# Kernel tuning notes

Hardware: AMD Instinct MI355X
Metric: run time of the kernel (lower is better)

Reference implementation:

```python
import jax, jax.numpy as jnp
import numpy as np

N_ATOMS = 512
N_SAMPLES = 2 ** 15  # 32768
N_ITER = 64


def time_domain_to_real(x):
    # rfft then concat(real, imag) along last dim -> length 2*(N//2+1)
    s = jnp.fft.rfft(x, axis=-1)
    return jnp.concatenate([s.real, s.imag], axis=-1)


def real_to_time_domain(x):
    half = x.shape[-1] // 2
    c = x[..., :half] + 1j * x[..., half:]
    return jnp.fft.irfft(c, axis=-1)  # n = 2*(half-1) = N_SAMPLES


def setup_inputs() -> dict:
    key = jax.random.key(0)
    k1, k2 = jax.random.split(key)
    x = jax.random.normal(k1, (64, 1, N_SAMPLES), dtype=jnp.float32)
    # learned atoms, initialized exactly as in Model.__init__
    env = jnp.linspace(1.0, 0.0, N_SAMPLES, dtype=jnp.float32) ** 12
    atoms_td = jax.random.uniform(k2, (1, N_ATOMS, N_SAMPLES), dtype=jnp.float32,
                                  minval=-0.01, maxval=0.01) * env[None, None, :]
    atoms = time_domain_to_real(atoms_td)  # (1, N_ATOMS, 32770)
    return {"x": x, "atoms": atoms}


def reference(x, atoms):
    xr = time_domain_to_real(x)            # (B, 1, L), L = 32770
    an = atoms / jnp.linalg.norm(atoms, axis=-1, keepdims=True)  # unit_norm over last axis
    an = an[0]                             # (A, L)
    res0 = xr[:, 0, :]                     # (B, L)
    rec0 = jnp.zeros_like(res0)

    def step(carry, _):
        res, rec = carry
        # sum(atoms * residual, -1) == dot products -> avoid (B,A,L) intermediate
        dots = jnp.einsum('bl,al->ba', res, an)      # (B, A)
        idx = jnp.argmax(dots, axis=1)               # (B,)
        best = an[idx] * res                         # take_along_dim(corr) == atoms[idx]*res
        return (res - best, rec + best), None

    (res, rec), _ = jax.lax.scan(step, (res0, rec0), None, length=N_ITER)
    reconstruction = real_to_time_domain(rec[:, None, :])  # (B, 1, N_SAMPLES)
    return reconstruction, res[:, None, :]
```

## Files before the change

kernel.cpp:

```cpp
#include <hip/hip_runtime.h>
#include <math.h>

#define NSAMP 32768
#define MH    16384
#define LFREQ 32770
#define NRE   16385
#define NB    64
#define NA    512
#define NITER 64
#define RSTR  32772

#define KPS    33280
#define NSL    64
#define BN2    128
#define USLICE 8
#define NCH    4097

typedef __attribute__((ext_vector_type(8))) short bf16x8;
typedef __attribute__((ext_vector_type(8))) unsigned short u16x8;
typedef __attribute__((ext_vector_type(4))) float f32x4;

__device__ __forceinline__ int rev4_14(int v) {
  unsigned r = __brev((unsigned)v) >> 18;
  r = ((r & 0x1555u) << 1) | ((r >> 1) & 0x1555u);
  return (int)r;
}

__device__ __forceinline__ unsigned short f2bf(float f) {
  unsigned u = __float_as_uint(f);
  u = (u + 0x7fffu + ((u >> 16) & 1u)) >> 16;
  return (unsigned short)u;
}
__device__ __forceinline__ float bf2f(unsigned short h) {
  return __uint_as_float(((unsigned)h) << 16);
}

__device__ __forceinline__ float2 cmul(float2 a, float2 b) {
  return make_float2(a.x * b.x - a.y * b.y, a.x * b.y + a.y * b.x);
}

__global__ __launch_bounds__(1024) void fft_fwd_kernel(const float* __restrict__ x,
                                                       float* __restrict__ res0,
                                                       unsigned short* __restrict__ resH,
                                                       unsigned short* __restrict__ resL) {
  extern __shared__ float2 s[];
  const int b = blockIdx.x, t = threadIdx.x;
  const float2* xrow = (const float2*)(x + (size_t)b * NSAMP);
  for (int m = t; m < MH; m += 1024) s[m] = xrow[rev4_14(m)];
  __syncthreads();
  for (int st = 0; st < 7; ++st) {
    const int q = 1 << (2 * st);
    const float fac = 6.283185307179586f / (float)(4 * q);
    for (int j = t; j < MH / 4; j += 1024) {
      const int blk = j >> (2 * st), pos = j & (q - 1);
      const int i0 = (blk << (2 * st + 2)) + pos;
      float sn, cs; __sincosf(fac * (float)pos, &sn, &cs);
      const float2 w1 = make_float2(cs, -sn);
      const float2 w2 = cmul(w1, w1);
      const float2 w3 = cmul(w2, w1);
      const float2 a0 = s[i0], a1 = s[i0 + q], a2 = s[i0 + 2 * q], a3 = s[i0 + 3 * q];
      const float2 x1 = cmul(w1, a1), x2 = cmul(w2, a2), x3 = cmul(w3, a3);
      const float2 s0 = make_float2(a0.x + x2.x, a0.y + x2.y);
      const float2 s1 = make_float2(a0.x - x2.x, a0.y - x2.y);
      const float2 t0 = make_float2(x1.x + x3.x, x1.y + x3.y);
      const float2 t1 = make_float2(x1.x - x3.x, x1.y - x3.y);
      s[i0]         = make_float2(s0.x + t0.x, s0.y + t0.y);
      s[i0 + q]     = make_float2(s1.x + t1.y, s1.y - t1.x);
      s[i0 + 2 * q] = make_float2(s0.x - t0.x, s0.y - t0.y);
      s[i0 + 3 * q] = make_float2(s1.x - t1.y, s1.y + t1.x);
    }
    __syncthreads();
  }
  float* rr = res0 + (size_t)b * RSTR;
  unsigned short* hrow = resH + (size_t)b * KPS;
  unsigned short* lrow = resL + (size_t)b * KPS;
  const float fac2 = 6.283185307179586f / (float)NSAMP;
  for (int k = t; k < MH; k += 1024) {
    if (k == 0) {
      const float2 z0 = s[0];
      const float dc = z0.x + z0.y, ny = z0.x - z0.y;
      rr[0] = dc;   rr[NRE] = 0.f;
      rr[MH] = ny;  rr[NRE + MH] = 0.f;
      unsigned short h;
      h = f2bf(dc); hrow[0] = h;  lrow[0] = f2bf(dc - bf2f(h));
      h = f2bf(ny); hrow[MH] = h; lrow[MH] = f2bf(ny - bf2f(h));
      hrow[NRE] = 0; lrow[NRE] = 0;
      hrow[NRE + MH] = 0; lrow[NRE + MH] = 0;
    } else {
      const float2 zk = s[k], zm = s[MH - k];
      const float xer = 0.5f * (zk.x + zm.x), xei = 0.5f * (zk.y - zm.y);
      const float p = 0.5f * (zk.y + zm.y);
      const float q = -0.5f * (zk.x - zm.x);
      float sn, cs; __sincosf(fac2 * (float)k, &sn, &cs);
      const float vr = xer + cs * p + sn * q;
      const float vi = xei + cs * q - sn * p;
      rr[k]       = vr;
      rr[NRE + k] = vi;
      unsigned short h;
      h = f2bf(vr); hrow[k] = h;       lrow[k] = f2bf(vr - bf2f(h));
      h = f2bf(vi); hrow[NRE + k] = h; lrow[NRE + k] = f2bf(vi - bf2f(h));
    }
  }
}

__global__ __launch_bounds__(1024) void fft_inv_kernel(const float* __restrict__ rec,
                                                       float* __restrict__ out) {
  extern __shared__ float2 s[];
  const int b = blockIdx.x, t = threadIdx.x;
  const float* rr = rec + (size_t)b * RSTR;
  const float fac2 = 6.283185307179586f / (float)NSAMP;
  for (int m = t; m < MH; m += 1024) {
    const int k = rev4_14(m);
    float2 z;
    if (k == 0) {
      const float a0 = rr[0], aM = rr[MH];
      z = make_float2(0.5f * (a0 + aM), 0.5f * (a0 - aM));
    } else {
      const float xr_ = rr[k],       xi_ = rr[NRE + k];
      const float mr  = rr[MH - k],  mi  = rr[NRE + MH - k];
      const float xer = 0.5f * (xr_ + mr), xei = 0.5f * (xi_ - mi);
      const float er  = 0.5f * (xr_ - mr), ei  = 0.5f * (xi_ + mi);
      float sn, cs; __sincosf(fac2 * (float)k, &sn, &cs);
      const float xor_ = cs * er - sn * ei;
      const float xoi  = cs * ei + sn * er;
      z = make_float2(xer - xoi, xei + xor_);
    }
    s[m] = z;
  }
  __syncthreads();
  for (int st = 0; st < 7; ++st) {
    const int q = 1 << (2 * st);
    const float fac = 6.283185307179586f / (float)(4 * q);
    for (int j = t; j < MH / 4; j += 1024) {
      const int blk = j >> (2 * st), pos = j & (q - 1);
      const int i0 = (blk << (2 * st + 2)) + pos;
      float sn, cs; __sincosf(fac * (float)pos, &sn, &cs);
      const float2 w1 = make_float2(cs, sn);
      const float2 w2 = cmul(w1, w1);
      const float2 w3 = cmul(w2, w1);
      const float2 a0 = s[i0], a1 = s[i0 + q], a2 = s[i0 + 2 * q], a3 = s[i0 + 3 * q];
      const float2 x1 = cmul(w1, a1), x2 = cmul(w2, a2), x3 = cmul(w3, a3);
      const float2 s0 = make_float2(a0.x + x2.x, a0.y + x2.y);
      const float2 s1 = make_float2(a0.x - x2.x, a0.y - x2.y);
      const float2 t0 = make_float2(x1.x + x3.x, x1.y + x3.y);
      const float2 t1 = make_float2(x1.x - x3.x, x1.y - x3.y);
      s[i0]         = make_float2(s0.x + t0.x, s0.y + t0.y);
      s[i0 + q]     = make_float2(s1.x - t1.y, s1.y + t1.x);
      s[i0 + 2 * q] = make_float2(s0.x - t0.x, s0.y - t0.y);
      s[i0 + 3 * q] = make_float2(s1.x + t1.y, s1.y - t1.x);
    }
    __syncthreads();
  }
  const float inv = 1.0f / (float)MH;
  float2* orow = (float2*)(out + (size_t)b * NSAMP);
  for (int m = t; m < MH; m += 1024) {
    const float2 z = s[m];
    orow[m] = make_float2(z.x * inv, z.y * inv);
  }
}

__global__ __launch_bounds__(256) void atom_norm_kernel(const float* __restrict__ atoms,
                                                        float* __restrict__ rnorm,
                                                        float* __restrict__ anv) {
  const int a = blockIdx.x, t = threadIdx.x;
  const float2* row2 = (const float2*)(atoms + (size_t)a * LFREQ);
  float ss = 0.f;
  for (int i = t; i < LFREQ / 2; i += 256) {
    const float2 v = row2[i];
    ss += v.x * v.x + v.y * v.y;
  }
  __shared__ float red[256];
  red[t] = ss; __syncthreads();
  for (int st = 128; st > 0; st >>= 1) {
    if (t < st) red[t] += red[t + st];
    __syncthreads();
  }
  if (t == 0) {
    const float rn = 1.0f / sqrtf(red[0]);
    rnorm[a] = rn;
    anv[a] = atoms[(size_t)a * LFREQ + 32768] * rn;
  }
}

__global__ __launch_bounds__(256) void an_bf16_kernel(const float* __restrict__ atoms,
                                                      const float* __restrict__ rnorm,
                                                      unsigned short* __restrict__ anH,
                                                      unsigned short* __restrict__ anL) {
  const int quarter = blockIdx.x;
  const int a = blockIdx.y;
  const int t = threadIdx.x;
  const float rn = rnorm[a];
  const float* row = atoms + (size_t)a * LFREQ;
  unsigned short* hrow = anH + (size_t)a * KPS;
  unsigned short* lrow = anL + (size_t)a * KPS;
  const int c0 = quarter * 1040;
  const int c1 = min(c0 + 1040, KPS / 8);
  for (int c = c0 + t; c < c1; c += 256) {
    const int k0 = c * 8;
    float v[8];
    if (k0 + 8 <= LFREQ) {
      #pragma unroll
      for (int e = 0; e < 4; ++e) {
        const float2 p = *(const float2*)(row + k0 + 2 * e);
        v[2 * e] = p.x; v[2 * e + 1] = p.y;
      }
    } else {
      #pragma unroll
      for (int e = 0; e < 8; ++e) v[e] = (k0 + e < LFREQ) ? row[k0 + e] : 0.f;
    }
    u16x8 hv, lv;
    #pragma unroll
    for (int e = 0; e < 8; ++e) {
      const float sv = v[e] * rn;
      const unsigned short h = f2bf(sv);
      hv[e] = h;
      lv[e] = f2bf(sv - bf2f(h));
    }
    *(u16x8*)(hrow + k0) = hv;
    *(u16x8*)(lrow + k0) = lv;
  }
}

__global__ __launch_bounds__(512) void dots_mfma_kernel(const unsigned short* __restrict__ resH,
                                                        const unsigned short* __restrict__ resL,
                                                        const unsigned short* __restrict__ anH,
                                                        const unsigned short* __restrict__ anL,
                                                        float* __restrict__ partials) {
  __shared__ char smem[98304];
  const int slice = blockIdx.x;
  const int atile = blockIdx.y;
  const int t = threadIdx.x;
  const int w = t >> 6, l = t & 63;
  const int bh = w >> 2, aq = w & 3;
  const int kc0 = slice * 512;

  f32x4 acc00 = {0.f,0.f,0.f,0.f}, acc01 = acc00, acc10 = acc00, acc11 = acc00;

#define STAGE(cc, bb)                                                                     \
  {                                                                                       \
    const int kc = kc0 + (cc) * 64;                                                       \
    _Pragma("unroll")                                                                     \
    for (int j = 0; j < 6; ++j) {                                                         \
      const int u = w * 6 + j;                                                            \
      const unsigned short* gt = (u < 8) ? resH : (u < 16) ? resL : (u < 32) ? anH : anL; \
      const int base = (u < 8) ? 0 : (u < 16) ? 8192 : (u < 32) ? 16384 : 32768;          \
      const int usec = u - ((u < 8) ? 0 : (u < 16) ? 8 : (u < 32) ? 16 : 32);             \
      const int row0 = (u < 16) ? 0 : atile * BN2;                                        \
      const int rt = usec >> 1, kk = usec & 1;                                            \
      const unsigned short* g = gt + (size_t)(row0 + rt * 16 + (l & 15)) * KPS            \
                                + kc + kk * 32 + (l >> 4) * 8;                            \
      char* d = smem + (bb) * 49152 + base + usec * 1024 + l * 16;                        \
      __builtin_amdgcn_global_load_lds((const __attribute__((address_space(1))) void*)g,  \
                                       (__attribute__((address_space(3))) void*)d,        \
                                       16, 0, 0);                                        \
    }                                                                                     \
  }

#define COMPUTE(bb)                                                                      \
  {                                                                                       \
    const char* base = smem + (bb) * 49152;                                               \
    _Pragma("unroll")                                                                     \
    for (int kk = 0; kk < 2; ++kk) {                                                      \
      const bf16x8 aH0 = *(const bf16x8*)(base + ((bh * 2 + 0) * 2 + kk) * 1024 + l * 16);\
      const bf16x8 aH1 = *(const bf16x8*)(base + ((bh * 2 + 1) * 2 + kk) * 1024 + l * 16);\
      const bf16x8 aL0 = *(const bf16x8*)(base + 8192 + ((bh * 2 + 0) * 2 + kk) * 1024 + l * 16);\
      const bf16x8 aL1 = *(const bf16x8*)(base + 8192 + ((bh * 2 + 1) * 2 + kk) * 1024 + l * 16);\
      const bf16x8 bH0 = *(const bf16x8*)(base + 16384 + ((aq * 2 + 0) * 2 + kk) * 1024 + l * 16);\
      const bf16x8 bH1 = *(const bf16x8*)(base + 16384 + ((aq * 2 + 1) * 2 + kk) * 1024 + l * 16);\
      const bf16x8 bL0 = *(const bf16x8*)(base + 32768 + ((aq * 2 + 0) * 2 + kk) * 1024 + l * 16);\
      const bf16x8 bL1 = *(const bf16x8*)(base + 32768 + ((aq * 2 + 1) * 2 + kk) * 1024 + l * 16);\
      acc00 = __builtin_amdgcn_mfma_f32_16x16x32_bf16(aH0, bH0, acc00, 0, 0, 0);          \
      acc01 = __builtin_amdgcn_mfma_f32_16x16x32_bf16(aH0, bH1, acc01, 0, 0, 0);          \
      acc10 = __builtin_amdgcn_mfma_f32_16x16x32_bf16(aH1, bH0, acc10, 0, 0, 0);          \
      acc11 = __builtin_amdgcn_mfma_f32_16x16x32_bf16(aH1, bH1, acc11, 0, 0, 0);          \
      acc00 = __builtin_amdgcn_mfma_f32_16x16x32_bf16(aH0, bL0, acc00, 0, 0, 0);          \
      acc01 = __builtin_amdgcn_mfma_f32_16x16x32_bf16(aH0, bL1, acc01, 0, 0, 0);          \
      acc10 = __builtin_amdgcn_mfma_f32_16x16x32_bf16(aH1, bL0, acc10, 0, 0, 0);          \
      acc11 = __builtin_amdgcn_mfma_f32_16x16x32_bf16(aH1, bL1, acc11, 0, 0, 0);          \
      acc00 = __builtin_amdgcn_mfma_f32_16x16x32_bf16(aL0, bH0, acc00, 0, 0, 0);          \
      acc01 = __builtin_amdgcn_mfma_f32_16x16x32_bf16(aL0, bH1, acc01, 0, 0, 0);          \
      acc10 = __builtin_amdgcn_mfma_f32_16x16x32_bf16(aL1, bH0, acc10, 0, 0, 0);          \
      acc11 = __builtin_amdgcn_mfma_f32_16x16x32_bf16(aL1, bH1, acc11, 0, 0, 0);          \
    }                                                                                     \
  }

  STAGE(0, 0);
  #pragma unroll
  for (int c = 0; c < 8; ++c) {
    const int buf = c & 1;
    if (c < 7) {
      STAGE(c + 1, buf ^ 1);
      asm volatile("s_waitcnt vmcnt(6)" ::: "memory");
    } else {
      asm volatile("s_waitcnt vmcnt(0)" ::: "memory");
    }
    __builtin_amdgcn_s_barrier();
    __builtin_amdgcn_sched_barrier(0);
    COMPUTE(buf);
    __builtin_amdgcn_sched_barrier(0);
    __builtin_amdgcn_s_barrier();
  }
#undef STAGE
#undef COMPUTE

  const int acol = atile * BN2 + aq * 32 + (l & 15);
  const size_t bstr = (size_t)NSL * NA;
  #pragma unroll
  for (int e = 0; e < 4; ++e) {
    const size_t r0 = (size_t)(bh * 32 + (l >> 4) * 4 + e);
    partials[r0 * bstr + (size_t)slice * NA + acol]             = acc00[e];
    partials[r0 * bstr + (size_t)slice * NA + acol + 16]        = acc01[e];
    partials[(r0 + 16) * bstr + (size_t)slice * NA + acol]      = acc10[e];
    partials[(r0 + 16) * bstr + (size_t)slice * NA + acol + 16] = acc11[e];
  }
}

__global__ __launch_bounds__(256) void reduce_argmax_kernel(const float* __restrict__ partials,
                                                            const unsigned short* __restrict__ resH,
                                                            const unsigned short* __restrict__ resL,
                                                            const float* __restrict__ anv,
                                                            int* __restrict__ bestidx) {
  const int b = blockIdx.x, t = threadIdx.x;
  const float* pb = partials + (size_t)b * NSL * NA;
  float d0 = 0.f, d1 = 0.f;
  #pragma unroll 16
  for (int s = 0; s < NSL; ++s) {
    d0 += pb[(size_t)s * NA + t];
    d1 += pb[(size_t)s * NA + t + 256];
  }
  const float rv = bf2f(resH[(size_t)b * KPS + 32768]) +
                   bf2f(resL[(size_t)b * KPS + 32768]);
  d0 = fmaf(rv, anv[t], d0);
  d1 = fmaf(rv, anv[t + 256], d1);
  float best = d0; int bi = t;
  if (d1 > best) { best = d1; bi = t + 256; }
  __shared__ float sv[256]; __shared__ int si[256];
  sv[t] = best; si[t] = bi; __syncthreads();
  for (int st = 128; st > 0; st >>= 1) {
    if (t < st) {
      const float v2 = sv[t + st]; const int i2 = si[t + st];
      if (v2 > sv[t] || (v2 == sv[t] && i2 < si[t])) { sv[t] = v2; si[t] = i2; }
    }
    __syncthreads();
  }
  if (t == 0) bestidx[b] = si[0];
}

__global__ __launch_bounds__(256) void update_kernel(const float* __restrict__ atoms,
                                                     const float* __restrict__ rnorm,
                                                     const int* __restrict__ bestidx,
                                                     unsigned short* __restrict__ resH,
                                                     unsigned short* __restrict__ resL,
                                                     const float* __restrict__ res0,
                                                     float* __restrict__ rec,
                                                     float* __restrict__ out2,
                                                     int final_out) {
  const int slice = blockIdx.x;
  const int b = blockIdx.y;
  const int t = threadIdx.x;
  const int idx = bestidx[b];
  const float rn = rnorm[idx];
  const float* arow = atoms + (size_t)idx * LFREQ;
  unsigned short* hrow = resH + (size_t)b * KPS;
  unsigned short* lrow = resL + (size_t)b * KPS;
  const float* r0row = res0 + (size_t)b * RSTR;
  float* recrow = rec + (size_t)b * RSTR;
  float* orow = out2 + (size_t)b * LFREQ;
  const int c0 = slice * 513;
  const int c1 = min(c0 + 513, NCH);
  for (int c = c0 + t; c < c1; c += 256) {
    const int k0 = c * 8;
    if (k0 + 8 <= LFREQ) {
      const u16x8 hv0 = *(const u16x8*)(hrow + k0);
      const u16x8 lv0 = *(const u16x8*)(lrow + k0);
      float av[8];
      #pragma unroll
      for (int e = 0; e < 4; ++e) {
        const float2 p = *(const float2*)(arow + k0 + 2 * e);
        av[2 * e] = p.x; av[2 * e + 1] = p.y;
      }
      float nv[8];
      u16x8 hv, lv;
      #pragma unroll
      for (int e = 0; e < 8; ++e) {
        const float r = bf2f(hv0[e]) + bf2f(lv0[e]);
        const float bx = av[e] * rn * r;
        nv[e] = r - bx;
        const unsigned short h = f2bf(nv[e]);
        hv[e] = h;
        lv[e] = f2bf(nv[e] - bf2f(h));
      }
      *(u16x8*)(hrow + k0) = hv;
      *(u16x8*)(lrow + k0) = lv;
      if (final_out) {
        #pragma unroll
        for (int e = 0; e < 2; ++e) {
          const float4 r0 = *(const float4*)(r0row + k0 + 4 * e);
          *(float4*)(orow + k0 + 4 * e) = make_float4(nv[4*e], nv[4*e+1], nv[4*e+2], nv[4*e+3]);
          *(float4*)(recrow + k0 + 4 * e) = make_float4(r0.x - nv[4*e], r0.y - nv[4*e+1],
                                                       r0.z - nv[4*e+2], r0.w - nv[4*e+3]);
        }
      }
    } else {
      for (int e = 0; e < 8; ++e) {
        const int k = k0 + e;
        if (k < LFREQ) {
          const float r = bf2f(hrow[k]) + bf2f(lrow[k]);
          const float bx = arow[k] * rn * r;
          const float nx = r - bx;
          const unsigned short h = f2bf(nx);
          hrow[k] = h;
          lrow[k] = f2bf(nx - bf2f(h));
          if (final_out) {
            orow[k] = nx;
            recrow[k] = r0row[k] - nx;
          }
        }
      }
    }
  }
}

extern "C" void kernel_launch(void* const* d_in, const int* in_sizes, int n_in,
                              void* d_out, int out_size, void* d_ws, size_t ws_size,
                              hipStream_t stream) {
  const float* x = (const float*)d_in[0];
  const float* atoms = (const float*)d_in[1];
  float* out = (float*)d_out;

  float* res0 = (float*)d_ws;
  float* rec = res0 + (size_t)NB * RSTR;
  float* rnorm = rec + (size_t)NB * RSTR;
  float* anv = rnorm + NA;
  float* partials = anv + NA;
  int* bestidx = (int*)(partials + (size_t)NB * NSL * NA);
  unsigned short* resH = (unsigned short*)(bestidx + 64);
  unsigned short* resL = resH + (size_t)NB * KPS;
  unsigned short* anH  = resL + (size_t)NB * KPS;
  unsigned short* anL  = anH + (size_t)NA * KPS;

  atom_norm_kernel<<<NA, 256, 0, stream>>>(atoms, rnorm, anv);
  an_bf16_kernel<<<dim3(4, NA), 256, 0, stream>>>(atoms, rnorm, anH, anL);
  fft_fwd_kernel<<<NB, 1024, MH * sizeof(float2), stream>>>(x, res0, resH, resL);

  float* res_out = out + (size_t)NB * NSAMP;
  for (int it = 0; it < NITER; ++it) {
    dots_mfma_kernel<<<dim3(NSL, 4), 512, 0, stream>>>(resH, resL, anH, anL, partials);
    reduce_argmax_kernel<<<NB, 256, 0, stream>>>(partials, resH, resL, anv, bestidx);
    update_kernel<<<dim3(USLICE, NB), 256, 0, stream>>>(atoms, rnorm, bestidx,
                                                        resH, resL, res0, rec, res_out,
                                                        (it == NITER - 1) ? 1 : 0);
  }

  fft_inv_kernel<<<NB, 1024, MH * sizeof(float2), stream>>>(rec, out);
}
```

Before: 1.832 ms.

## Triple-buffer dots staging, merge prologue kernels, widen argmax reduction

The MFMA dot kernel moves from double to triple buffering in LDS (96KB to 144KB). It now issues stages two ahead and drops the trailing barrier, so loads overlap compute with fewer syncs. The atom-norm, bf16-split and forward FFT kernels are merged into one prologue launch with separate block roles. The per-iteration reduce/argmax kernel uses 1024 threads, splitting the partial-sum loop across two halves. The larger LDS footprint limits occupancy of the dots kernel to one block per CU, and removing the barrier relies on the three-buffer rotation to avoid overwriting data still being read.

```diff
diff --git a/kernel.cpp b/kernel.cpp
--- a/kernel.cpp
+++ b/kernel.cpp
@@ -39,12 +39,66 @@
   return make_float2(a.x * b.x - a.y * b.y, a.x * b.y + a.y * b.x);
 }
 
-__global__ __launch_bounds__(1024) void fft_fwd_kernel(const float* __restrict__ x,
-                                                       float* __restrict__ res0,
-                                                       unsigned short* __restrict__ resH,
-                                                       unsigned short* __restrict__ resL) {
+__global__ __launch_bounds__(1024) void prologue_kernel(const float* __restrict__ x,
+                                                        float* __restrict__ res0,
+                                                        unsigned short* __restrict__ resH,
+                                                        unsigned short* __restrict__ resL,
+                                                        const float* __restrict__ atoms,
+                                                        float* __restrict__ rnorm,
+                                                        float* __restrict__ anv,
+                                                        unsigned short* __restrict__ anH,
+                                                        unsigned short* __restrict__ anL) {
   extern __shared__ float2 s[];
-  const int b = blockIdx.x, t = threadIdx.x;
+  const int t = threadIdx.x;
+  if (blockIdx.x >= 64) {
+    const int a = blockIdx.x - 64;
+    float* red = (float*)s;
+    const float* row = atoms + (size_t)a * LFREQ;
+    const float2* row2 = (const float2*)row;
+    float ss = 0.f;
+    for (int i = t; i < LFREQ / 2; i += 1024) {
+      const float2 v = row2[i];
+      ss += v.x * v.x + v.y * v.y;
+    }
+    red[t] = ss; __syncthreads();
+    for (int st = 512; st > 0; st >>= 1) {
+      if (t < st) red[t] += red[t + st];
+      __syncthreads();
+    }
+    const float rn = 1.0f / sqrtf(red[0]);
+    if (t == 0) {
+      rnorm[a] = rn;
+      anv[a] = atoms[(size_t)a * LFREQ + 32768] * rn;
+    }
+    unsigned short* hrow = anH + (size_t)a * KPS;
+    unsigned short* lrow = anL + (size_t)a * KPS;
+    for (int c = t; c < KPS / 8; c += 1024) {
+      const int k0 = c * 8;
+      float v[8];
+      if (k0 + 8 <= LFREQ) {
+        #pragma unroll
+        for (int e = 0; e < 4; ++e) {
+          const float2 p = *(const float2*)(row + k0 + 2 * e);
+          v[2 * e] = p.x; v[2 * e + 1] = p.y;
+        }
+      } else {
+        #pragma unroll
+        for (int e = 0; e < 8; ++e) v[e] = (k0 + e < LFREQ) ? row[k0 + e] : 0.f;
+      }
+      u16x8 hv, lv;
+      #pragma unroll
+      for (int e = 0; e < 8; ++e) {
+        const float sv = v[e] * rn;
+        const unsigned short h = f2bf(sv);
+        hv[e] = h;
+        lv[e] = f2bf(sv - bf2f(h));
+      }
+      *(u16x8*)(hrow + k0) = hv;
+      *(u16x8*)(lrow + k0) = lv;
+    }
+    return;
+  }
+  const int b = blockIdx.x;
   const float2* xrow = (const float2*)(x + (size_t)b * NSAMP);
   for (int m = t; m < MH; m += 1024) s[m] = xrow[rev4_14(m)];
   __syncthreads();
@@ -159,74 +213,12 @@
   }
 }
 
-__global__ __launch_bounds__(256) void atom_norm_kernel(const float* __restrict__ atoms,
-                                                        float* __restrict__ rnorm,
-                                                        float* __restrict__ anv) {
-  const int a = blockIdx.x, t = threadIdx.x;
-  const float2* row2 = (const float2*)(atoms + (size_t)a * LFREQ);
-  float ss = 0.f;
-  for (int i = t; i < LFREQ / 2; i += 256) {
-    const float2 v = row2[i];
-    ss += v.x * v.x + v.y * v.y;
-  }
-  __shared__ float red[256];
-  red[t] = ss; __syncthreads();
-  for (int st = 128; st > 0; st >>= 1) {
-    if (t < st) red[t] += red[t + st];
-    __syncthreads();
-  }
-  if (t == 0) {
-    const float rn = 1.0f / sqrtf(red[0]);
-    rnorm[a] = rn;
-    anv[a] = atoms[(size_t)a * LFREQ + 32768] * rn;
-  }
-}
-
-__global__ __launch_bounds__(256) void an_bf16_kernel(const float* __restrict__ atoms,
-                                                      const float* __restrict__ rnorm,
-                                                      unsigned short* __restrict__ anH,
-                                                      unsigned short* __restrict__ anL) {
-  const int quarter = blockIdx.x;
-  const int a = blockIdx.y;
-  const int t = threadIdx.x;
-  const float rn = rnorm[a];
-  const float* row = atoms + (size_t)a * LFREQ;
-  unsigned short* hrow = anH + (size_t)a * KPS;
-  unsigned short* lrow = anL + (size_t)a * KPS;
-  const int c0 = quarter * 1040;
-  const int c1 = min(c0 + 1040, KPS / 8);
-  for (int c = c0 + t; c < c1; c += 256) {
-    const int k0 = c * 8;
-    float v[8];
-    if (k0 + 8 <= LFREQ) {
-      #pragma unroll
-      for (int e = 0; e < 4; ++e) {
-        const float2 p = *(const float2*)(row + k0 + 2 * e);
-        v[2 * e] = p.x; v[2 * e + 1] = p.y;
-      }
-    } else {
-      #pragma unroll
-      for (int e = 0; e < 8; ++e) v[e] = (k0 + e < LFREQ) ? row[k0 + e] : 0.f;
-    }
-    u16x8 hv, lv;
-    #pragma unroll
-    for (int e = 0; e < 8; ++e) {
-      const float sv = v[e] * rn;
-      const unsigned short h = f2bf(sv);
-      hv[e] = h;
-      lv[e] = f2bf(sv - bf2f(h));
-    }
-    *(u16x8*)(hrow + k0) = hv;
-    *(u16x8*)(lrow + k0) = lv;
-  }
-}
-
 __global__ __launch_bounds__(512) void dots_mfma_kernel(const unsigned short* __restrict__ resH,
                                                         const unsigned short* __restrict__ resL,
                                                         const unsigned short* __restrict__ anH,
                                                         const unsigned short* __restrict__ anL,
                                                         float* __restrict__ partials) {
-  __shared__ char smem[98304];
+  __shared__ char smem[147456];
   const int slice = blockIdx.x;
   const int atile = blockIdx.y;
   const int t = threadIdx.x;
@@ -285,20 +277,23 @@
   }
 
   STAGE(0, 0);
+  STAGE(1, 1);
   #pragma unroll
   for (int c = 0; c < 8; ++c) {
-    const int buf = c & 1;
+    const int bf = c - (c / 3) * 3;
     if (c < 7) {
-      STAGE(c + 1, buf ^ 1);
       asm volatile("s_waitcnt vmcnt(6)" ::: "memory");
     } else {
       asm volatile("s_waitcnt vmcnt(0)" ::: "memory");
     }
     __builtin_amdgcn_s_barrier();
     __builtin_amdgcn_sched_barrier(0);
-    COMPUTE(buf);
+    COMPUTE(bf);
     __builtin_amdgcn_sched_barrier(0);
-    __builtin_amdgcn_s_barrier();
+    if (c < 6) {
+      const int nb = c + 2;
+      STAGE(nb, nb - (nb / 3) * 3);
+    }
   }
 #undef STAGE
 #undef COMPUTE
@@ -315,28 +310,29 @@
   }
 }
 
-__global__ __launch_bounds__(256) void reduce_argmax_kernel(const float* __restrict__ partials,
-                                                            const unsigned short* __restrict__ resH,
-                                                            const unsigned short* __restrict__ resL,
-                                                            const float* __restrict__ anv,
-                                                            int* __restrict__ bestidx) {
+__global__ __launch_bounds__(1024) void reduce_argmax_kernel(const float* __restrict__ partials,
+                                                             const unsigned short* __restrict__ resH,
+                                                             const unsigned short* __restrict__ resL,
+                                                             const float* __restrict__ anv,
+                                                             int* __restrict__ bestidx) {
   const int b = blockIdx.x, t = threadIdx.x;
-  const float* pb = partials + (size_t)b * NSL * NA;
-  float d0 = 0.f, d1 = 0.f;
+  const int a = t & 511, half = t >> 9;
+  const float* pb = partials + (size_t)b * NSL * NA + (size_t)half * 32 * NA;
+  float d = 0.f;
   #pragma unroll 16
-  for (int s = 0; s < NSL; ++s) {
-    d0 += pb[(size_t)s * NA + t];
-    d1 += pb[(size_t)s * NA + t + 256];
-  }
-  const float rv = bf2f(resH[(size_t)b * KPS + 32768]) +
-                   bf2f(resL[(size_t)b * KPS + 32768]);
-  d0 = fmaf(rv, anv[t], d0);
-  d1 = fmaf(rv, anv[t + 256], d1);
-  float best = d0; int bi = t;
-  if (d1 > best) { best = d1; bi = t + 256; }
-  __shared__ float sv[256]; __shared__ int si[256];
-  sv[t] = best; si[t] = bi; __syncthreads();
-  for (int st = 128; st > 0; st >>= 1) {
+  for (int s = 0; s < 32; ++s) d += pb[(size_t)s * NA + a];
+  __shared__ float sv[1024];
+  __shared__ int si[1024];
+  sv[t] = d; __syncthreads();
+  if (t < 512) {
+    float dd = sv[t] + sv[t + 512];
+    const float rv = bf2f(resH[(size_t)b * KPS + 32768]) +
+                     bf2f(resL[(size_t)b * KPS + 32768]);
+    dd = fmaf(rv, anv[t], dd);
+    sv[t] = dd; si[t] = t;
+  }
+  __syncthreads();
+  for (int st = 256; st > 0; st >>= 1) {
     if (t < st) {
       const float v2 = sv[t + st]; const int i2 = si[t + st];
       if (v2 > sv[t] || (v2 == sv[t] && i2 < si[t])) { sv[t] = v2; si[t] = i2; }
@@ -439,14 +435,14 @@
   unsigned short* anH  = resL + (size_t)NB * KPS;
   unsigned short* anL  = anH + (size_t)NA * KPS;
 
-  atom_norm_kernel<<<NA, 256, 0, stream>>>(atoms, rnorm, anv);
-  an_bf16_kernel<<<dim3(4, NA), 256, 0, stream>>>(atoms, rnorm, anH, anL);
-  fft_fwd_kernel<<<NB, 1024, MH * sizeof(float2), stream>>>(x, res0, resH, resL);
+  prologue_kernel<<<64 + NA, 1024, MH * sizeof(float2), stream>>>(x, res0, resH, resL,
+                                                                  atoms, rnorm, anv,
+                                                                  anH, anL);
 
   float* res_out = out + (size_t)NB * NSAMP;
   for (int it = 0; it < NITER; ++it) {
     dots_mfma_kernel<<<dim3(NSL, 4), 512, 0, stream>>>(resH, resL, anH, anL, partials);
-    reduce_argmax_kernel<<<NB, 256, 0, stream>>>(partials, resH, resL, anv, bestidx);
+    reduce_argmax_kernel<<<NB, 1024, 0, stream>>>(partials, resH, resL, anv, bestidx);
     update_kernel<<<dim3(USLICE, NB), 256, 0, stream>>>(atoms, rnorm, bestidx,
                                                         resH, resL, res0, rec, res_out,
                                                         (it == NITER - 1) ? 1 : 0);
```

Result: faster. 1.750 ms (median of 2 runs) (-4.5%).
